# Kernel tuning notes

Hardware: AMD Instinct MI355X
Metric: run time of the kernel (lower is better)

The kernel has to match this reference:

```python
import jax, jax.numpy as jnp
import numpy as np

B, T, D, H = 16, 2048, 1024, 64  # batch, seq_len(block_sz), emb_dim, head_sz


def setup_inputs() -> dict:
    key = jax.random.key(0)
    k0, k1, k2, k3 = jax.random.split(key, 4)
    x = jax.random.normal(k0, (B, T, D), dtype=jnp.float32)
    # nn.Linear(D, H, bias=False) weights, stored as [D, H] so y = x @ W
    s = 1.0 / np.sqrt(D)
    Wq = jax.random.uniform(k1, (D, H), dtype=jnp.float32, minval=-s, maxval=s)
    Wk = jax.random.uniform(k2, (D, H), dtype=jnp.float32, minval=-s, maxval=s)
    Wv = jax.random.uniform(k3, (D, H), dtype=jnp.float32, minval=-s, maxval=s)
    return {"x": x, "Wq": Wq, "Wk": Wk, "Wv": Wv}


def reference(x, Wq, Wk, Wv):
    # Single-head causal self-attention, naive (materializes full [B,T,T] scores).
    q = x @ Wq  # [B, T, H]
    k = x @ Wk  # [B, T, H]
    v = x @ Wv  # [B, T, H]
    scale = 1.0 / (q.shape[-1] ** 0.5)
    w = jnp.einsum("btd,bsd->bts", q, k) * scale  # [B, T, T]
    causal = jnp.tril(jnp.ones((T, T), dtype=bool))
    w = jnp.where(causal, w, -jnp.inf)
    w = jax.nn.softmax(w, axis=-1)
    # dropout p=0.0 -> identity
    out = jnp.einsum("bts,bsd->btd", w, v)  # [B, T, H]
    return out
```

## Files before the change

### kernel.cpp

```cpp
#include <hip/hip_runtime.h>
#include <math.h>

#define BB 16
#define TT 2048
#define DD 1024
#define HH 64
#define QK_SCALE 0.18033688011112042f

typedef short bf16x8 __attribute__((ext_vector_type(8)));
typedef short bf16x4 __attribute__((ext_vector_type(4)));
typedef float f32x4 __attribute__((ext_vector_type(4)));

__device__ __forceinline__ short f2bf(float f) {
  union { float f; unsigned u; } c; c.f = f;
  unsigned u = c.u + 0x7FFFu + ((c.u >> 16) & 1u);
  return (short)(u >> 16);
}
__device__ __forceinline__ short f2bf_up(float f) {
  union { float f; unsigned u; } c; c.f = f;
  return (short)((c.u + 0x8000u) >> 16);
}

__device__ __forceinline__ void* lds_swz(void* base, int row, int col) {
  int byte = (row << 7) + (col << 1);
  byte ^= (row & 7) << 4;
  return (void*)((char*)base + byte);
}
__device__ __forceinline__ void* lds_swz256(void* base, int row, int col) {
  int byte = (row << 8) + (col << 1);
  byte ^= (row & 7) << 4;
  return (void*)((char*)base + byte);
}

__device__ __forceinline__ void pack16(const float4& a0, const float4& a1,
                                       const float4& a2, const float4& a3,
                                       bf16x8& s0, bf16x8& s1) {
  s0[0] = f2bf(a0.x); s0[1] = f2bf(a0.y); s0[2] = f2bf(a0.z); s0[3] = f2bf(a0.w);
  s0[4] = f2bf(a1.x); s0[5] = f2bf(a1.y); s0[6] = f2bf(a1.z); s0[7] = f2bf(a1.w);
  s1[0] = f2bf(a2.x); s1[1] = f2bf(a2.y); s1[2] = f2bf(a2.z); s1[3] = f2bf(a2.w);
  s1[4] = f2bf(a3.x); s1[5] = f2bf(a3.y); s1[6] = f2bf(a3.z); s1[7] = f2bf(a3.w);
}

__global__ __launch_bounds__(256) void pack_wt(
    const float* __restrict__ Wq, const float* __restrict__ Wk,
    const float* __restrict__ Wv, short* __restrict__ wt) {
  const int idx = blockIdx.x * 256 + threadIdx.x;
  const int n = idx >> 7;
  const int k0 = (idx & 127) << 3;
  const float* W = (n < 64) ? Wq : (n < 128) ? Wk : Wv;
  const int h = n & 63;
  bf16x8 o;
#pragma unroll
  for (int j = 0; j < 8; ++j) o[j] = f2bf(W[(k0 + j) * HH + h]);
  *(bf16x8*)&wt[n * DD + k0] = o;
}

__global__ __launch_bounds__(256) void qkv_mfma(
    const float* __restrict__ x, const short* __restrict__ wt,
    short* __restrict__ qo, short* __restrict__ ko, short* __restrict__ vt) {
  __shared__ short xs[2][64 * 64];
  const int tid = threadIdx.x;
  const int lane = tid & 63;
  const int w = tid >> 6;
  const int q16 = lane & 15;
  const int g = lane >> 4;
  const size_t r0 = (size_t)blockIdx.x * 64;

  const int srow = tid >> 2;
  const int sc = (tid & 3) << 4;
  const float* xrow = x + (r0 + srow) * DD + sc;

  f32x4 acc[4][3];
#pragma unroll
  for (int mf = 0; mf < 4; ++mf)
#pragma unroll
    for (int nf = 0; nf < 3; ++nf) acc[mf][nf] = (f32x4){0.f, 0.f, 0.f, 0.f};

  const short* wp[3];
#pragma unroll
  for (int nf = 0; nf < 3; ++nf)
    wp[nf] = wt + (size_t)(w * 48 + nf * 16 + q16) * DD + g * 8;

  {
    const float4* xp = (const float4*)xrow;
    float4 a0 = xp[0], a1 = xp[1], a2 = xp[2], a3 = xp[3];
    bf16x8 s0, s1;
    pack16(a0, a1, a2, a3, s0, s1);
    *(bf16x8*)lds_swz(xs[0], srow, sc) = s0;
    *(bf16x8*)lds_swz(xs[0], srow, sc + 8) = s1;
  }
  bf16x8 bcur[3][2];
#pragma unroll
  for (int nf = 0; nf < 3; ++nf)
#pragma unroll
    for (int kf = 0; kf < 2; ++kf)
      bcur[nf][kf] = *(const bf16x8*)(wp[nf] + kf * 32);
  __syncthreads();

  int cur = 0;
  for (int ks = 0; ks < 16; ++ks) {
    float4 a0, a1, a2, a3;
    bf16x8 bnxt[3][2];
    if (ks < 15) {
      const int k1 = (ks + 1) << 6;
      const float4* xp = (const float4*)(xrow + k1);
      a0 = xp[0]; a1 = xp[1]; a2 = xp[2]; a3 = xp[3];
#pragma unroll
      for (int nf = 0; nf < 3; ++nf)
#pragma unroll
        for (int kf = 0; kf < 2; ++kf)
          bnxt[nf][kf] = *(const bf16x8*)(wp[nf] + k1 + kf * 32);
    }

    bf16x8 afr[4][2];
#pragma unroll
    for (int mf = 0; mf < 4; ++mf)
#pragma unroll
      for (int kf = 0; kf < 2; ++kf)
        afr[mf][kf] = *(bf16x8*)lds_swz(xs[cur], mf * 16 + q16, kf * 32 + g * 8);

#pragma unroll
    for (int mf = 0; mf < 4; ++mf)
#pragma unroll
      for (int nf = 0; nf < 3; ++nf)
#pragma unroll
        for (int kf = 0; kf < 2; ++kf)
          acc[mf][nf] = __builtin_amdgcn_mfma_f32_16x16x32_bf16(
              afr[mf][kf], bcur[nf][kf], acc[mf][nf], 0, 0, 0);

    if (ks < 15) {
      bf16x8 s0, s1;
      pack16(a0, a1, a2, a3, s0, s1);
      *(bf16x8*)lds_swz(xs[cur ^ 1], srow, sc) = s0;
      *(bf16x8*)lds_swz(xs[cur ^ 1], srow, sc + 8) = s1;
      __syncthreads();
      cur ^= 1;
#pragma unroll
      for (int nf = 0; nf < 3; ++nf)
#pragma unroll
        for (int kf = 0; kf < 2; ++kf) bcur[nf][kf] = bnxt[nf][kf];
    }
  }

#pragma unroll
  for (int nf = 0; nf < 3; ++nf) {
    const int n = w * 48 + nf * 16 + q16;
    const int mat = n >> 6;
    const int h = n & 63;
    if (mat < 2) {
      short* outp = mat ? ko : qo;
      const float fac = mat ? 1.0f : QK_SCALE;
#pragma unroll
      for (int mf = 0; mf < 4; ++mf)
#pragma unroll
        for (int r = 0; r < 4; ++r)
          outp[(r0 + mf * 16 + g * 4 + r) * HH + h] = f2bf(acc[mf][nf][r] * fac);
    } else {
      const int bb = (int)(r0 >> 11);
      const int tloc = (int)(r0 & 2047);
#pragma unroll
      for (int mf = 0; mf < 4; ++mf) {
        bf16x4 pk;
#pragma unroll
        for (int r = 0; r < 4; ++r) pk[r] = f2bf(acc[mf][nf][r]);
        *(bf16x4*)&vt[((size_t)bb * HH + h) * TT + tloc + mf * 16 + g * 4] = pk;
      }
    }
  }
}

__global__ __launch_bounds__(512) void attn_mfma(
    const short* __restrict__ q, const short* __restrict__ k,
    const short* __restrict__ vt, float* __restrict__ out) {
  __shared__ short klds[2][128 * 64];
  __shared__ short vlds[2][64 * 128];
  __shared__ short ps[8][16 * 136];

  const int p = blockIdx.x;
  const int b = blockIdx.y;
  const int tid = threadIdx.x;
  const int lane = tid & 63;
  const int w = tid >> 6;
  const int grp = w >> 2;
  const int wl = w & 3;
  const int q16 = lane & 15;
  const int g = lane >> 4;

  const int qt = grp ? (31 - p) : p;
  const int t0 = qt << 6;
  const int NC = (33 - p) >> 1;
  const int cmax = (qt * 64 + 63) >> 7;
  const int qrow = t0 + wl * 16 + g * 4;

  const size_t brow = (size_t)b * TT;
  const short* kg = k + brow * HH;
  const short* vtg = vt + (size_t)b * HH * TT;

  const int srow2 = tid >> 2;
  const int scq = (tid & 3) << 4;
  const int vrow = tid >> 3;
  const int vcol = (tid & 7) << 4;

  bf16x8 kr0 = *(const bf16x8*)&kg[srow2 * HH + scq];
  bf16x8 kr1 = *(const bf16x8*)&kg[srow2 * HH + scq + 8];
  bf16x8 vr0 = *(const bf16x8*)&vtg[vrow * TT + vcol];
  bf16x8 vr1 = *(const bf16x8*)&vtg[vrow * TT + vcol + 8];

  {
    const int qtrow = (srow2 < 64) ? ((p << 6) + srow2)
                                   : (((31 - p) << 6) + (srow2 - 64));
    const short* qsrc = q + (brow + qtrow) * HH;
    *(bf16x8*)lds_swz(klds[0], srow2, scq) = *(const bf16x8*)&qsrc[scq];
    *(bf16x8*)lds_swz(klds[0], srow2, scq + 8) = *(const bf16x8*)&qsrc[scq + 8];
  }
  __syncthreads();
  bf16x8 qa[2];
#pragma unroll
  for (int kf = 0; kf < 2; ++kf)
    qa[kf] = *(bf16x8*)lds_swz(klds[0], grp * 64 + wl * 16 + q16, kf * 32 + g * 8);
  __syncthreads();

  *(bf16x8*)lds_swz(klds[0], srow2, scq) = kr0;
  *(bf16x8*)lds_swz(klds[0], srow2, scq + 8) = kr1;
  *(bf16x8*)lds_swz256(vlds[0], vrow, vcol) = vr0;
  *(bf16x8*)lds_swz256(vlds[0], vrow, vcol + 8) = vr1;
  __syncthreads();

  f32x4 po[4];
  f32x4 lacc = (f32x4){0.f, 0.f, 0.f, 0.f};
  float m[4];
#pragma unroll
  for (int nf = 0; nf < 4; ++nf) po[nf] = (f32x4){0.f, 0.f, 0.f, 0.f};
#pragma unroll
  for (int r = 0; r < 4; ++r) m[r] = -INFINITY;

  const bf16x8 ones = {0x3F80, 0x3F80, 0x3F80, 0x3F80,
                       0x3F80, 0x3F80, 0x3F80, 0x3F80};
  int cur = 0;

  for (int c = 0; c < NC; ++c) {
    const bool notlast = (c + 1 < NC);
    if (notlast) {
      const int s1 = (c + 1) << 7;
      kr0 = *(const bf16x8*)&kg[(s1 + srow2) * HH + scq];
      kr1 = *(const bf16x8*)&kg[(s1 + srow2) * HH + scq + 8];
      vr0 = *(const bf16x8*)&vtg[vrow * TT + s1 + vcol];
      vr1 = *(const bf16x8*)&vtg[vrow * TT + s1 + vcol + 8];
    }

    if (c <= cmax) {
      f32x4 sfr[8];
#pragma unroll
      for (int nf = 0; nf < 8; ++nf) sfr[nf] = (f32x4){0.f, 0.f, 0.f, 0.f};
#pragma unroll
      for (int nf = 0; nf < 8; ++nf)
#pragma unroll
        for (int kf = 0; kf < 2; ++kf) {
          bf16x8 kb = *(bf16x8*)lds_swz(klds[cur], nf * 16 + q16, kf * 32 + g * 8);
          sfr[nf] = __builtin_amdgcn_mfma_f32_16x16x32_bf16(qa[kf], kb, sfr[nf], 0, 0, 0);
        }

      if (c == cmax) {
        const int sbase = (c << 7) + q16;
#pragma unroll
        for (int nf = 0; nf < 8; ++nf)
#pragma unroll
          for (int r = 0; r < 4; ++r)
            if (sbase + nf * 16 > qrow + r) sfr[nf][r] = -INFINITY;
      }

      float pm[4];
#pragma unroll
      for (int r = 0; r < 4; ++r) {
        float a = fmaxf(fmaxf(sfr[0][r], sfr[1][r]), fmaxf(sfr[2][r], sfr[3][r]));
        float bx = fmaxf(fmaxf(sfr[4][r], sfr[5][r]), fmaxf(sfr[6][r], sfr[7][r]));
        pm[r] = fmaxf(a, bx);
      }
#pragma unroll
      for (int off = 8; off; off >>= 1)
#pragma unroll
        for (int r = 0; r < 4; ++r) pm[r] = fmaxf(pm[r], __shfl_xor(pm[r], off));

      float growth = fmaxf(fmaxf(pm[0] - m[0], pm[1] - m[1]),
                           fmaxf(pm[2] - m[2], pm[3] - m[3]));
      if (__any(growth > 8.f)) {
#pragma unroll
        for (int r = 0; r < 4; ++r) {
          const float mn = fmaxf(m[r], pm[r]);
          const float corr = exp2f(m[r] - mn);
          m[r] = mn;
          lacc[r] *= corr;
#pragma unroll
          for (int nf = 0; nf < 4; ++nf) po[nf][r] *= corr;
        }
      }

#pragma unroll
      for (int nf = 0; nf < 8; ++nf)
#pragma unroll
        for (int r = 0; r < 4; ++r)
          ps[w][(g * 4 + r) * 136 + nf * 16 + q16] = f2bf_up(exp2f(sfr[nf][r] - m[r]));

      bf16x8 pa[4];
#pragma unroll
      for (int kf = 0; kf < 4; ++kf)
        pa[kf] = *(const bf16x8*)&ps[w][q16 * 136 + kf * 32 + g * 8];
#pragma unroll
      for (int nf = 0; nf < 4; ++nf)
#pragma unroll
        for (int kf = 0; kf < 4; ++kf) {
          bf16x8 vb = *(bf16x8*)lds_swz256(vlds[cur], nf * 16 + q16, kf * 32 + g * 8);
          po[nf] = __builtin_amdgcn_mfma_f32_16x16x32_bf16(pa[kf], vb, po[nf], 0, 0, 0);
        }
#pragma unroll
      for (int kf = 0; kf < 4; ++kf)
        lacc = __builtin_amdgcn_mfma_f32_16x16x32_bf16(pa[kf], ones, lacc, 0, 0, 0);
    }

    if (notlast) {
      *(bf16x8*)lds_swz(klds[cur ^ 1], srow2, scq) = kr0;
      *(bf16x8*)lds_swz(klds[cur ^ 1], srow2, scq + 8) = kr1;
      *(bf16x8*)lds_swz256(vlds[cur ^ 1], vrow, vcol) = vr0;
      *(bf16x8*)lds_swz256(vlds[cur ^ 1], vrow, vcol + 8) = vr1;
      __syncthreads();
      cur ^= 1;
    }
  }

#pragma unroll
  for (int nf = 0; nf < 4; ++nf) {
    const int h = nf * 16 + q16;
#pragma unroll
    for (int r = 0; r < 4; ++r)
      out[(brow + qrow + r) * HH + h] = po[nf][r] / lacc[r];
  }
}

extern "C" void kernel_launch(void* const* d_in, const int* in_sizes, int n_in,
                              void* d_out, int out_size, void* d_ws, size_t ws_size,
                              hipStream_t stream) {
  const float* x  = (const float*)d_in[0];
  const float* Wq = (const float*)d_in[1];
  const float* Wk = (const float*)d_in[2];
  const float* Wv = (const float*)d_in[3];
  float* out = (float*)d_out;

  const size_t bth = (size_t)BB * TT * HH;
  short* qb  = (short*)d_ws;
  short* kb  = qb + bth;
  short* vtb = kb + bth;
  short* wtb = vtb + bth;

  pack_wt<<<96, 256, 0, stream>>>(Wq, Wk, Wv, wtb);
  qkv_mfma<<<(BB * TT) / 64, 256, 0, stream>>>(x, wtb, qb, kb, vtb);
  attn_mfma<<<dim3(16, BB), 512, 0, stream>>>(qb, kb, vtb, out);
}
```

Baseline: 86.80 us.

## Split attention blocks to 256 threads single-buffered LDS with more resident blocks

Restructures the attention kernel from 512-thread blocks handling two paired query tiles with double-buffered K/V LDS into 256-thread blocks each handling one 64-row query tile. LDS is single-buffered so more blocks fit per CU (launch bounds 256,3), and load balance is handled by reversing the tile order by batch index. It also wraps MFMA sections in s_setprio to favor matrix issue. The cost is an extra barrier per chunk, since the LDS stores no longer overlap compute, and per-block work is now more uneven.

```diff
diff --git a/kernel.cpp b/kernel.cpp
--- a/kernel.cpp
+++ b/kernel.cpp
@@ -169,61 +169,60 @@
   }
 }
 
-__global__ __launch_bounds__(512) void attn_mfma(
+__global__ __launch_bounds__(256, 3) void attn_mfma(
     const short* __restrict__ q, const short* __restrict__ k,
     const short* __restrict__ vt, float* __restrict__ out) {
-  __shared__ short klds[2][128 * 64];
-  __shared__ short vlds[2][64 * 128];
-  __shared__ short ps[8][16 * 136];
-
-  const int p = blockIdx.x;
+  __shared__ short klds[128 * 64];
+  __shared__ short vlds[64 * 128];
+  __shared__ short ps[4][16 * 136];
+
+  const int bx = blockIdx.x;
   const int b = blockIdx.y;
+  const int qt = (b >= 8) ? bx : (31 - bx);
+  const int t0 = qt << 6;
   const int tid = threadIdx.x;
   const int lane = tid & 63;
   const int w = tid >> 6;
-  const int grp = w >> 2;
-  const int wl = w & 3;
   const int q16 = lane & 15;
   const int g = lane >> 4;
-
-  const int qt = grp ? (31 - p) : p;
-  const int t0 = qt << 6;
-  const int NC = (33 - p) >> 1;
-  const int cmax = (qt * 64 + 63) >> 7;
-  const int qrow = t0 + wl * 16 + g * 4;
+  const int NC = (qt >> 1) + 1;
+  const int qrow = t0 + w * 16 + g * 4;
 
   const size_t brow = (size_t)b * TT;
   const short* kg = k + brow * HH;
   const short* vtg = vt + (size_t)b * HH * TT;
 
-  const int srow2 = tid >> 2;
-  const int scq = (tid & 3) << 4;
-  const int vrow = tid >> 3;
-  const int vcol = (tid & 7) << 4;
-
-  bf16x8 kr0 = *(const bf16x8*)&kg[srow2 * HH + scq];
-  bf16x8 kr1 = *(const bf16x8*)&kg[srow2 * HH + scq + 8];
-  bf16x8 vr0 = *(const bf16x8*)&vtg[vrow * TT + vcol];
-  bf16x8 vr1 = *(const bf16x8*)&vtg[vrow * TT + vcol + 8];
+  const int krow = tid >> 1;
+  const int kcol = (tid & 1) << 5;
+  const int vrow = tid >> 2;
+  const int vcol = (tid & 3) << 5;
+
+  bf16x8 kr[4], vr[4];
+#pragma unroll
+  for (int j = 0; j < 4; ++j) {
+    kr[j] = *(const bf16x8*)&kg[krow * HH + kcol + j * 8];
+    vr[j] = *(const bf16x8*)&vtg[vrow * TT + vcol + j * 8];
+  }
 
   {
-    const int qtrow = (srow2 < 64) ? ((p << 6) + srow2)
-                                   : (((31 - p) << 6) + (srow2 - 64));
-    const short* qsrc = q + (brow + qtrow) * HH;
-    *(bf16x8*)lds_swz(klds[0], srow2, scq) = *(const bf16x8*)&qsrc[scq];
-    *(bf16x8*)lds_swz(klds[0], srow2, scq + 8) = *(const bf16x8*)&qsrc[scq + 8];
+    const int qsr = tid >> 2;
+    const int qsc = (tid & 3) << 4;
+    const short* qsrc = q + (brow + t0 + qsr) * HH;
+    *(bf16x8*)lds_swz(vlds, qsr, qsc) = *(const bf16x8*)&qsrc[qsc];
+    *(bf16x8*)lds_swz(vlds, qsr, qsc + 8) = *(const bf16x8*)&qsrc[qsc + 8];
   }
   __syncthreads();
   bf16x8 qa[2];
 #pragma unroll
   for (int kf = 0; kf < 2; ++kf)
-    qa[kf] = *(bf16x8*)lds_swz(klds[0], grp * 64 + wl * 16 + q16, kf * 32 + g * 8);
+    qa[kf] = *(bf16x8*)lds_swz(vlds, w * 16 + q16, kf * 32 + g * 8);
   __syncthreads();
 
-  *(bf16x8*)lds_swz(klds[0], srow2, scq) = kr0;
-  *(bf16x8*)lds_swz(klds[0], srow2, scq + 8) = kr1;
-  *(bf16x8*)lds_swz256(vlds[0], vrow, vcol) = vr0;
-  *(bf16x8*)lds_swz256(vlds[0], vrow, vcol + 8) = vr1;
+#pragma unroll
+  for (int j = 0; j < 4; ++j) {
+    *(bf16x8*)lds_swz(klds, krow, kcol + j * 8) = kr[j];
+    *(bf16x8*)lds_swz256(vlds, vrow, vcol + j * 8) = vr[j];
+  }
   __syncthreads();
 
   f32x4 po[4];
@@ -236,94 +235,97 @@
 
   const bf16x8 ones = {0x3F80, 0x3F80, 0x3F80, 0x3F80,
                        0x3F80, 0x3F80, 0x3F80, 0x3F80};
-  int cur = 0;
 
   for (int c = 0; c < NC; ++c) {
     const bool notlast = (c + 1 < NC);
     if (notlast) {
       const int s1 = (c + 1) << 7;
-      kr0 = *(const bf16x8*)&kg[(s1 + srow2) * HH + scq];
-      kr1 = *(const bf16x8*)&kg[(s1 + srow2) * HH + scq + 8];
-      vr0 = *(const bf16x8*)&vtg[vrow * TT + s1 + vcol];
-      vr1 = *(const bf16x8*)&vtg[vrow * TT + s1 + vcol + 8];
-    }
-
-    if (c <= cmax) {
-      f32x4 sfr[8];
-#pragma unroll
-      for (int nf = 0; nf < 8; ++nf) sfr[nf] = (f32x4){0.f, 0.f, 0.f, 0.f};
+#pragma unroll
+      for (int j = 0; j < 4; ++j) {
+        kr[j] = *(const bf16x8*)&kg[(s1 + krow) * HH + kcol + j * 8];
+        vr[j] = *(const bf16x8*)&vtg[vrow * TT + s1 + vcol + j * 8];
+      }
+    }
+
+    f32x4 sfr[8];
+#pragma unroll
+    for (int nf = 0; nf < 8; ++nf) sfr[nf] = (f32x4){0.f, 0.f, 0.f, 0.f};
+    __builtin_amdgcn_s_setprio(1);
+#pragma unroll
+    for (int nf = 0; nf < 8; ++nf)
+#pragma unroll
+      for (int kf = 0; kf < 2; ++kf) {
+        bf16x8 kb = *(bf16x8*)lds_swz(klds, nf * 16 + q16, kf * 32 + g * 8);
+        sfr[nf] = __builtin_amdgcn_mfma_f32_16x16x32_bf16(qa[kf], kb, sfr[nf], 0, 0, 0);
+      }
+    __builtin_amdgcn_s_setprio(0);
+
+    if (c == NC - 1) {
+      const int sbase = (c << 7) + q16;
 #pragma unroll
       for (int nf = 0; nf < 8; ++nf)
 #pragma unroll
-        for (int kf = 0; kf < 2; ++kf) {
-          bf16x8 kb = *(bf16x8*)lds_swz(klds[cur], nf * 16 + q16, kf * 32 + g * 8);
-          sfr[nf] = __builtin_amdgcn_mfma_f32_16x16x32_bf16(qa[kf], kb, sfr[nf], 0, 0, 0);
-        }
-
-      if (c == cmax) {
-        const int sbase = (c << 7) + q16;
-#pragma unroll
-        for (int nf = 0; nf < 8; ++nf)
-#pragma unroll
-          for (int r = 0; r < 4; ++r)
-            if (sbase + nf * 16 > qrow + r) sfr[nf][r] = -INFINITY;
-      }
-
-      float pm[4];
+        for (int r = 0; r < 4; ++r)
+          if (sbase + nf * 16 > qrow + r) sfr[nf][r] = -INFINITY;
+    }
+
+    float pm[4];
+#pragma unroll
+    for (int r = 0; r < 4; ++r) {
+      float a = fmaxf(fmaxf(sfr[0][r], sfr[1][r]), fmaxf(sfr[2][r], sfr[3][r]));
+      float bx2 = fmaxf(fmaxf(sfr[4][r], sfr[5][r]), fmaxf(sfr[6][r], sfr[7][r]));
+      pm[r] = fmaxf(a, bx2);
+    }
+#pragma unroll
+    for (int off = 8; off; off >>= 1)
+#pragma unroll
+      for (int r = 0; r < 4; ++r) pm[r] = fmaxf(pm[r], __shfl_xor(pm[r], off));
+
+    float growth = fmaxf(fmaxf(pm[0] - m[0], pm[1] - m[1]),
+                         fmaxf(pm[2] - m[2], pm[3] - m[3]));
+    if (__any(growth > 8.f)) {
 #pragma unroll
       for (int r = 0; r < 4; ++r) {
-        float a = fmaxf(fmaxf(sfr[0][r], sfr[1][r]), fmaxf(sfr[2][r], sfr[3][r]));
-        float bx = fmaxf(fmaxf(sfr[4][r], sfr[5][r]), fmaxf(sfr[6][r], sfr[7][r]));
-        pm[r] = fmaxf(a, bx);
-      }
-#pragma unroll
-      for (int off = 8; off; off >>= 1)
-#pragma unroll
-        for (int r = 0; r < 4; ++r) pm[r] = fmaxf(pm[r], __shfl_xor(pm[r], off));
-
-      float growth = fmaxf(fmaxf(pm[0] - m[0], pm[1] - m[1]),
-                           fmaxf(pm[2] - m[2], pm[3] - m[3]));
-      if (__any(growth > 8.f)) {
-#pragma unroll
-        for (int r = 0; r < 4; ++r) {
-          const float mn = fmaxf(m[r], pm[r]);
-          const float corr = exp2f(m[r] - mn);
-          m[r] = mn;
-          lacc[r] *= corr;
-#pragma unroll
-          for (int nf = 0; nf < 4; ++nf) po[nf][r] *= corr;
-        }
-      }
-
-#pragma unroll
-      for (int nf = 0; nf < 8; ++nf)
-#pragma unroll
-        for (int r = 0; r < 4; ++r)
-          ps[w][(g * 4 + r) * 136 + nf * 16 + q16] = f2bf_up(exp2f(sfr[nf][r] - m[r]));
-
-      bf16x8 pa[4];
-#pragma unroll
-      for (int kf = 0; kf < 4; ++kf)
-        pa[kf] = *(const bf16x8*)&ps[w][q16 * 136 + kf * 32 + g * 8];
-#pragma unroll
-      for (int nf = 0; nf < 4; ++nf)
-#pragma unroll
-        for (int kf = 0; kf < 4; ++kf) {
-          bf16x8 vb = *(bf16x8*)lds_swz256(vlds[cur], nf * 16 + q16, kf * 32 + g * 8);
-          po[nf] = __builtin_amdgcn_mfma_f32_16x16x32_bf16(pa[kf], vb, po[nf], 0, 0, 0);
-        }
-#pragma unroll
-      for (int kf = 0; kf < 4; ++kf)
-        lacc = __builtin_amdgcn_mfma_f32_16x16x32_bf16(pa[kf], ones, lacc, 0, 0, 0);
-    }
+        const float mn = fmaxf(m[r], pm[r]);
+        const float corr = exp2f(m[r] - mn);
+        m[r] = mn;
+        lacc[r] *= corr;
+#pragma unroll
+        for (int nf = 0; nf < 4; ++nf) po[nf][r] *= corr;
+      }
+    }
+
+#pragma unroll
+    for (int nf = 0; nf < 8; ++nf)
+#pragma unroll
+      for (int r = 0; r < 4; ++r)
+        ps[w][(g * 4 + r) * 136 + nf * 16 + q16] = f2bf_up(exp2f(sfr[nf][r] - m[r]));
+
+    bf16x8 pa[4];
+#pragma unroll
+    for (int kf = 0; kf < 4; ++kf)
+      pa[kf] = *(const bf16x8*)&ps[w][q16 * 136 + kf * 32 + g * 8];
+    __builtin_amdgcn_s_setprio(1);
+#pragma unroll
+    for (int nf = 0; nf < 4; ++nf)
+#pragma unroll
+      for (int kf = 0; kf < 4; ++kf) {
+        bf16x8 vb = *(bf16x8*)lds_swz256(vlds, nf * 16 + q16, kf * 32 + g * 8);
+        po[nf] = __builtin_amdgcn_mfma_f32_16x16x32_bf16(pa[kf], vb, po[nf], 0, 0, 0);
+      }
+#pragma unroll
+    for (int kf = 0; kf < 4; ++kf)
+      lacc = __builtin_amdgcn_mfma_f32_16x16x32_bf16(pa[kf], ones, lacc, 0, 0, 0);
+    __builtin_amdgcn_s_setprio(0);
 
     if (notlast) {
-      *(bf16x8*)lds_swz(klds[cur ^ 1], srow2, scq) = kr0;
-      *(bf16x8*)lds_swz(klds[cur ^ 1], srow2, scq + 8) = kr1;
-      *(bf16x8*)lds_swz256(vlds[cur ^ 1], vrow, vcol) = vr0;
-      *(bf16x8*)lds_swz256(vlds[cur ^ 1], vrow, vcol + 8) = vr1;
       __syncthreads();
-      cur ^= 1;
+#pragma unroll
+      for (int j = 0; j < 4; ++j) {
+        *(bf16x8*)lds_swz(klds, krow, kcol + j * 8) = kr[j];
+        *(bf16x8*)lds_swz256(vlds, vrow, vcol + j * 8) = vr[j];
+      }
+      __syncthreads();
     }
   }
 
@@ -353,5 +355,5 @@
 
   pack_wt<<<96, 256, 0, stream>>>(Wq, Wk, Wv, wtb);
   qkv_mfma<<<(BB * TT) / 64, 256, 0, stream>>>(x, wtb, qb, kb, vtb);
-  attn_mfma<<<dim3(16, BB), 512, 0, stream>>>(qb, kb, vtb, out);
-}
+  attn_mfma<<<dim3(32, BB), 256, 0, stream>>>(qb, kb, vtb, out);
+}
```

Result: no change. 86.84 us (+0.0%).
